# Performance work log

Hardware: AMD Instinct MI355X
Metric: run time of the kernel (lower is better)

## Reference

```python
import jax, jax.numpy as jnp
import numpy as np

HID, NQ, NKV, HD = 4096, 32, 8, 128
EPS = 1e-6
GOLDEN = 1.618033988749895
BASE = 10000.0


def _rmsnorm(x, w, eps=EPS):
    var = jnp.mean(x.astype(jnp.float32) ** 2, axis=-1, keepdims=True)
    return (x * jax.lax.rsqrt(var + eps)).astype(x.dtype) * w


def _rope_half(t, pos, inv_freq):
    # t: (B,T,H,dh); pos: (B,T); inv_freq: (dh//2,)
    ang = pos.astype(jnp.float32)[..., None] * inv_freq  # (B,T,dq)
    cos = jnp.cos(ang)[:, :, None, :]
    sin = jnp.sin(ang)[:, :, None, :]
    dq = inv_freq.shape[0]
    t1, t2 = t[..., :dq], t[..., dq:]
    return jnp.concatenate([t1 * cos - t2 * sin, t1 * sin + t2 * cos], axis=-1)


def _apply_ggrope(q, k, row_ids, col_ids):
    # 2D RoPE: first half of head_dim encodes rows, second half encodes cols;
    # column frequencies scaled by the golden ratio (GGRoPE).
    dh = HD // 2
    inv_freq = 1.0 / (BASE ** (jnp.arange(0, dh, 2, dtype=jnp.float32) / dh))
    inv_freq_col = inv_freq * GOLDEN

    def rot(t):
        tr = _rope_half(t[..., :dh], row_ids, inv_freq)
        tc = _rope_half(t[..., dh:], col_ids, inv_freq_col)
        return jnp.concatenate([tr, tc], axis=-1)

    return rot(q), rot(k)


def setup_inputs() -> dict:
    key = jax.random.key(0)
    ks = jax.random.split(key, 9)
    B, T = 1, 2048
    s = 0.02
    return {
        "x": jax.random.normal(ks[0], (B, T, HID), jnp.float32),
        "row_ids": jax.random.randint(ks[1], (B, T), 0, 30),
        "col_ids": jax.random.randint(ks[2], (B, T), 0, 30),
        "attention_mask": jnp.zeros((B, 1, T, T), jnp.float32),
        "Wq": jax.random.normal(ks[3], (HID, NQ * HD), jnp.float32) * s,
        "Wk": jax.random.normal(ks[4], (HID, NKV * HD), jnp.float32) * s,
        "Wv": jax.random.normal(ks[5], (HID, NKV * HD), jnp.float32) * s,
        "Wo": jax.random.normal(ks[6], (NQ * HD, HID), jnp.float32) * s,
        "q_norm_w": jnp.ones((HD,), jnp.float32),
        "k_norm_w": jnp.ones((HD,), jnp.float32),
    }


def reference(x, row_ids, col_ids, attention_mask, Wq, Wk, Wv, Wo, q_norm_w, k_norm_w):
    B, T, _ = x.shape
    group = NQ // NKV
    q = (x @ Wq).reshape(B, T, NQ, HD)
    k = (x @ Wk).reshape(B, T, NKV, HD)
    v = (x @ Wv).reshape(B, T, NKV, HD)
    q = _rmsnorm(q, q_norm_w)
    k = _rmsnorm(k, k_norm_w)
    q, k = _apply_ggrope(q, k, row_ids, col_ids)
    # expand KV heads to match query heads (GQA)
    k = jnp.repeat(k, group, axis=2)  # (B,T,NQ,HD)
    v = jnp.repeat(v, group, axis=2)
    q = q.transpose(0, 2, 1, 3)  # (B,NQ,T,HD)
    k = k.transpose(0, 2, 1, 3)
    v = v.transpose(0, 2, 1, 3)
    ssmax_scale = (HD ** -0.5) * np.log(max(T, 2)).astype(np.float32)
    scores = jnp.einsum("bhqd,bhkd->bhqk", q, k) * ssmax_scale
    scores = scores + attention_mask
    attn = jax.nn.softmax(scores.astype(jnp.float32), axis=-1).astype(q.dtype)
    out = jnp.einsum("bhqk,bhkd->bhqd", attn, v)
    out = out.transpose(0, 2, 1, 3).reshape(B, T, NQ * HD)
    return out @ Wo
```

## Files before the change

kernel.cpp:

```cpp
#include <hip/hip_runtime.h>
#include <hip/hip_bf16.h>

typedef unsigned short u16;
typedef __attribute__((ext_vector_type(8))) short bf16x8;
typedef __attribute__((ext_vector_type(4))) float f32x4;

#define LOG2E_F 1.4426950408889634f
#define QSCALE (0.08838834764831845f * 7.625595228825695f * 1.4426950408889634f)

__device__ __forceinline__ u16 f2bf(float f) {
  unsigned x = __float_as_uint(f);
  unsigned r = (x + 0x7fffu + ((x >> 16) & 1u)) >> 16;
  return (u16)r;
}
__device__ __forceinline__ float bf2f(u16 u) {
  return __uint_as_float(((unsigned)u) << 16);
}
__device__ __forceinline__ float exp2a(float x) {
  float r;
  asm("v_exp_f32 %0, %1" : "=v"(r) : "v"(x));
  return r;
}
__device__ __forceinline__ unsigned cvtpk(float lo, float hi) {
  unsigned r;
  asm("v_cvt_pk_bf16_f32 %0, %1, %2" : "=v"(r) : "v"(lo), "v"(hi));
  return r;
}

__device__ __forceinline__ void gload_lds16(const void* g, void* l) {
  __builtin_amdgcn_global_load_lds(
      (__attribute__((address_space(1))) void*)(g),
      (__attribute__((address_space(3))) void*)(l), 16, 0, 0);
}

__device__ __forceinline__ f32x4 mfma16(bf16x8 a, bf16x8 b, f32x4 c) {
  return __builtin_amdgcn_mfma_f32_16x16x32_bf16(a, b, c, 0, 0, 0);
}

__global__ __launch_bounds__(256) void cvt_x(const float4* __restrict__ x,
                                             ushort4* __restrict__ xb) {
  size_t i = (size_t)blockIdx.x * 256 + threadIdx.x;
  float4 v = x[i];
  ushort4 o;
  o.x = f2bf(v.x); o.y = f2bf(v.y); o.z = f2bf(v.z); o.w = f2bf(v.w);
  xb[i] = o;
}

__global__ __launch_bounds__(256) void tcvt(const float* __restrict__ src,
                                            u16* __restrict__ dst, int N) {
  __shared__ float t[64][65];
  int bid = blockIdx.x;
  int kt = bid & 63, nt = bid >> 6;
  int k0 = kt * 64, n0 = nt * 64;
  int tid = threadIdx.x;
#pragma unroll
  for (int it = 0; it < 16; ++it) {
    int idx = it * 256 + tid;
    int row = idx >> 6, col = idx & 63;
    t[row][col] = src[(size_t)(k0 + row) * N + n0 + col];
  }
  __syncthreads();
#pragma unroll
  for (int it = 0; it < 8; ++it) {
    int idx = it * 256 + tid;
    int nrow = idx >> 5, kc = idx & 31;
    ushort2 o;
    o.x = f2bf(t[kc * 2][nrow]);
    o.y = f2bf(t[kc * 2 + 1][nrow]);
    *(ushort2*)&dst[(size_t)(n0 + nrow) * 4096 + k0 + kc * 2] = o;
  }
}

__global__ __launch_bounds__(256) void maskflag(const float4* __restrict__ mask,
                                                int* __restrict__ flag) {
  size_t i = (size_t)blockIdx.x * 256 + threadIdx.x;
  float4 v = mask[i];
  if (v.x != 0.f || v.y != 0.f || v.z != 0.f || v.w != 0.f) atomicOr(flag, 1);
}

__global__ __launch_bounds__(256) void trig_kernel(const int* __restrict__ row_ids,
                                                   const int* __restrict__ col_ids,
                                                   float4* __restrict__ trig) {
  int idx = blockIdx.x * 256 + threadIdx.x;
  int tok = idx >> 5, i = idx & 31;
  float inv = exp2f(-(float)i * 0.41524101186092030f);
  float ar = (float)row_ids[tok] * inv;
  float ac = (float)col_ids[tok] * inv * 1.618033988749895f;
  float4 o;
  o.x = cosf(ar); o.y = sinf(ar); o.z = cosf(ac); o.w = sinf(ac);
  trig[idx] = o;
}

__global__ __launch_bounds__(256) void rope_kernel(u16* __restrict__ qk,
                                                   const float4* __restrict__ trig,
                                                   const float* __restrict__ qw,
                                                   const float* __restrict__ kw) {
  const int tok = blockIdx.x;
  const int tid = threadIdx.x;
  const int w = tid >> 6, lane = tid & 63;
  float4 t4 = trig[tok * 32 + (lane & 31)];
  float sgn = (lane < 32) ? -1.0f : 1.0f;

  for (int it = 0; it < 10; ++it) {
    int hh = w + it * 4;
    bool isQ = (hh < 32);
    int colbase = isQ ? hh * 128 : 4096 + (hh - 32) * 128;
    const float* nw = isQ ? qw : kw;
    float scale = isQ ? QSCALE : 1.0f;
    u16* p = qk + (size_t)tok * 5120 + colbase;
    float v1 = bf2f(p[lane]);
    float v2 = bf2f(p[64 + lane]);
    float w1 = nw[lane], w2 = nw[64 + lane];
    float ss = v1 * v1 + v2 * v2;
    ss += __shfl_xor(ss, 1);  ss += __shfl_xor(ss, 2);  ss += __shfl_xor(ss, 4);
    ss += __shfl_xor(ss, 8);  ss += __shfl_xor(ss, 16); ss += __shfl_xor(ss, 32);
    float rinv = rsqrtf(ss * (1.0f / 128.0f) + 1e-6f);
    float n1 = v1 * rinv * w1;
    float n2 = v2 * rinv * w2;
    float p1 = __shfl_xor(n1, 32);
    float p2 = __shfl_xor(n2, 32);
    float r1 = n1 * t4.x + sgn * p1 * t4.y;
    float r2 = n2 * t4.z + sgn * p2 * t4.w;
    p[lane]      = f2bf(r1 * scale);
    p[64 + lane] = f2bf(r2 * scale);
  }
}

template <int MODE>
__global__ __launch_bounds__(512, 2) void gemm256(const u16* __restrict__ A,
                                                  const u16* __restrict__ Bt,
                                                  void* __restrict__ C0,
                                                  u16* __restrict__ Vt, int nnt) {
  extern __shared__ char smem[];
  const int tid = threadIdx.x, lane = tid & 63, w = tid >> 6;
  const int l15 = lane & 15, l4 = lane >> 4;
  const int wr = w >> 2, wc = w & 3;
  constexpr int NF = (MODE == 0) ? 3 : 4;
  constexpr int BNW = (MODE == 0) ? 48 : 64;

  int wgid = (blockIdx.x & 7) * (gridDim.x >> 3) + (blockIdx.x >> 3);
  int kh = 0;
  if (MODE == 1) { kh = wgid >> 7; wgid &= 127; }
  const int mt = wgid / nnt, nt = wgid % nnt;
  const int m0 = mt * 256;
  const int n0 = nt * ((MODE == 0) ? 192 : 256);
  const int tbase = kh * 32;

  const int kswz = (((tid & 7) ^ ((tid >> 3) & 7)) << 4);
  const char* arow = (const char*)A + (size_t)(m0 + (tid >> 3)) * 8192 + kswz;
  const char* brow = (const char*)Bt + (size_t)(n0 + (tid >> 3)) * 8192 + kswz;

  auto stageA = [&](int t, int h) {
#pragma unroll
    for (int rd = 0; rd < 2; ++rd)
      gload_lds16(arow + (size_t)(h * 128 + rd * 64) * 8192 + t * 128,
                  smem + ((t & 1) * 2 + h) * 16384 + rd * 8192 + w * 1024);
  };
  auto stageB0 = [&](int t) {
#pragma unroll
    for (int rd = 0; rd < 3; ++rd)
      gload_lds16(brow + (size_t)(rd * 64) * 8192 + t * 128,
                  smem + 65536 + (t & 1) * 24576 + rd * 8192 + w * 1024);
  };
  auto stageB1 = [&](int t, int h) {
#pragma unroll
    for (int rd = 0; rd < 2; ++rd)
      gload_lds16(brow + (size_t)(h * 128 + rd * 64) * 8192 + t * 128,
                  smem + 65536 + ((t & 1) * 2 + h) * 16384 + rd * 8192 + w * 1024);
  };

  f32x4 acc[8][NF];
#pragma unroll
  for (int i = 0; i < 8; ++i)
#pragma unroll
    for (int j = 0; j < NF; ++j) acc[i][j] = (f32x4){0.f, 0.f, 0.f, 0.f};

  const int aoff0 = ((l4) ^ (l15 & 7)) << 4;
  const int aoff1 = ((4 + l4) ^ (l15 & 7)) << 4;

  stageA(tbase, 0); stageA(tbase, 1);
  if constexpr (MODE == 0) {
    stageB0(tbase); stageB0(tbase + 1);
    asm volatile("s_waitcnt vmcnt(3)" ::: "memory");
  } else {
    stageB1(tbase, 0); stageB1(tbase, 1);
    stageB1(tbase + 1, 0); stageB1(tbase + 1, 1);
    asm volatile("s_waitcnt vmcnt(4)" ::: "memory");
  }
  __builtin_amdgcn_s_barrier();

  auto do_iter = [&](int t0, int last) {
    bf16x8 bfr[NF][2];
#pragma unroll
    for (int p = 0; p < 8; ++p) {
      const int s = p >> 2, qd = p & 3;
      const char* aT = smem + (s * 2 + wr) * 16384 + l15 * 128;
      bf16x8 afr[2][2];
#pragma unroll
      for (int jm = 0; jm < 2; ++jm) {
        afr[jm][0] = *(const bf16x8*)(aT + (2 * qd + jm) * 2048 + aoff0);
        afr[jm][1] = *(const bf16x8*)(aT + (2 * qd + jm) * 2048 + aoff1);
      }
      if (qd == 0) {
        const char* bT;
        if constexpr (MODE == 0)
          bT = smem + 65536 + s * 24576 + (wc * 48 + l15) * 128;
        else
          bT = smem + 65536 + (s * 2 + (wc >> 1)) * 16384 +
               ((wc & 1) * 64 + l15) * 128;
#pragma unroll
        for (int nf = 0; nf < NF; ++nf) {
          bfr[nf][0] = *(const bf16x8*)(bT + nf * 2048 + aoff0);
          bfr[nf][1] = *(const bf16x8*)(bT + nf * 2048 + aoff1);
        }
      }
      if (p == 0) { stageA(t0 + 1, 0); stageA(t0 + 1, 1); }
      if (!last) {
        if constexpr (MODE == 0) {
          if (p == 1) stageB0(t0 + 2);
          if (p == 5) stageB0(t0 + 3);
        } else {
          if (p == 1) stageB1(t0 + 2, 0);
          if (p == 2) stageB1(t0 + 2, 1);
          if (p == 5) stageB1(t0 + 3, 0);
          if (p == 6) stageB1(t0 + 3, 1);
        }
        if (p == 4) { stageA(t0 + 2, 0); stageA(t0 + 2, 1); }
      }
      if (p == 3) {
        if (last) asm volatile("s_waitcnt vmcnt(0)" ::: "memory");
        else if constexpr (MODE == 0)
          asm volatile("s_waitcnt vmcnt(3)" ::: "memory");
        else
          asm volatile("s_waitcnt vmcnt(4)" ::: "memory");
      }
      if (p == 7 && !last) {
        if constexpr (MODE == 0)
          asm volatile("s_waitcnt vmcnt(3)" ::: "memory");
        else
          asm volatile("s_waitcnt vmcnt(4)" ::: "memory");
      }
      __builtin_amdgcn_s_barrier();
      asm volatile("s_waitcnt lgkmcnt(0)" ::: "memory");
      __builtin_amdgcn_sched_barrier(0);
      __builtin_amdgcn_s_setprio(1);
#pragma unroll
      for (int ks = 0; ks < 2; ++ks)
#pragma unroll
        for (int jm = 0; jm < 2; ++jm)
#pragma unroll
          for (int nf = 0; nf < NF; ++nf)
            acc[2 * qd + jm][nf] =
                mfma16(afr[jm][ks], bfr[nf][ks], acc[2 * qd + jm][nf]);
      __builtin_amdgcn_s_setprio(0);
      __builtin_amdgcn_s_barrier();
    }
  };

  constexpr int NIT = (MODE == 0) ? 32 : 16;
  for (int j = 0; j < NIT - 1; ++j) do_iter(tbase + 2 * j, 0);
  do_iter(tbase + 2 * (NIT - 1), 1);

  if (MODE == 0) {
    u16* qkp = (u16*)C0;
#pragma unroll
    for (int mf = 0; mf < 8; ++mf)
#pragma unroll
      for (int nf = 0; nf < NF; ++nf) {
        int ng = n0 + wc * BNW + nf * 16 + l15;
        if (ng < 5120) {
#pragma unroll
          for (int r = 0; r < 4; ++r) {
            int mg = m0 + wr * 128 + mf * 16 + l4 * 4 + r;
            qkp[(size_t)mg * 5120 + ng] = f2bf(acc[mf][nf][r]);
          }
        } else {
          int vr = ng - 5120;
          int mg = m0 + wr * 128 + mf * 16 + l4 * 4;
          ushort4 pk;
          pk.x = f2bf(acc[mf][nf][0]); pk.y = f2bf(acc[mf][nf][1]);
          pk.z = f2bf(acc[mf][nf][2]); pk.w = f2bf(acc[mf][nf][3]);
          *(ushort4*)&Vt[(size_t)vr * 2048 + mg] = pk;
        }
      }
  } else {
    float* Cp = (float*)C0 + (size_t)kh * 8388608;
#pragma unroll
    for (int mf = 0; mf < 8; ++mf)
#pragma unroll
      for (int nf = 0; nf < NF; ++nf) {
        int ng = n0 + wc * BNW + nf * 16 + l15;
#pragma unroll
        for (int r = 0; r < 4; ++r) {
          int mg = m0 + wr * 128 + mf * 16 + l4 * 4 + r;
          Cp[(size_t)mg * 4096 + ng] = acc[mf][nf][r];
        }
      }
  }
}

__global__ __launch_bounds__(256) void reduce2(const float4* __restrict__ p0,
                                               const float4* __restrict__ p1,
                                               float4* __restrict__ out) {
  size_t i = (size_t)blockIdx.x * 256 + threadIdx.x;
  float4 a = p0[i], b = p1[i];
  float4 o;
  o.x = a.x + b.x; o.y = a.y + b.y; o.z = a.z + b.z; o.w = a.w + b.w;
  out[i] = o;
}

__global__ __launch_bounds__(512, 2) void attn_kernel(const u16* __restrict__ qk,
                                                      const u16* __restrict__ vt,
                                                      u16* __restrict__ oat,
                                                      const float* __restrict__ mask,
                                                      const int* __restrict__ flag) {
  __shared__ u16 k_lds[2][64 * 128];
  __shared__ u16 v_lds[2][64 * 128];

  const int tid = threadIdx.x, lane = tid & 63, w = tid >> 6;
  const int l15 = lane & 15, l4 = lane >> 4;
  const int bid = blockIdx.x;
  const int hk = bid & 7;
  const int rest = bid >> 3;
  const int h = hk * 4 + (rest & 3);
  const int qt = rest >> 2;
  const int qbase = qt * 256 + w * 32;

  const bool use_mask = (*flag != 0);
  const char* kbase = (const char*)qk + 8192 + (size_t)hk * 256;
  const char* vbase = (const char*)vt + (size_t)hk * 128 * 4096;

  bf16x8 qf[2][4];
#pragma unroll
  for (int qg = 0; qg < 2; ++qg) {
    const char* qp = (const char*)qk +
                     (size_t)(qbase + qg * 16 + l15) * 10240 + h * 256 + l4 * 16;
#pragma unroll
    for (int ks = 0; ks < 4; ++ks) qf[qg][ks] = *(const bf16x8*)(qp + ks * 64);
  }

  f32x4 oacc[2][8];
#pragma unroll
  for (int qg = 0; qg < 2; ++qg)
#pragma unroll
    for (int fd = 0; fd < 8; ++fd) oacc[qg][fd] = (f32x4){0.f, 0.f, 0.f, 0.f};
  float m_run[2] = {-1e30f, -1e30f};
  float l_run[2] = {0.f, 0.f};

  int koff[4], voff[2];
#pragma unroll
  for (int ks = 0; ks < 4; ++ks) koff[ks] = ((4 * ks + l4) ^ l15) << 4;
#pragma unroll
  for (int ks = 0; ks < 2; ++ks) voff[ks] = ((4 * ks + l4) ^ (l15 & 7)) << 4;

#define STAGE(buf, kv0)                                                        \
  {                                                                            \
    _Pragma("unroll") for (int rd = 0; rd < 2; ++rd) {                         \
      int c = rd * 512 + tid;                                                  \
      int row = c >> 4;                                                        \
      int src = ((c & 15) ^ (row & 15)) << 4;                                  \
      gload_lds16(kbase + (size_t)((kv0) + row) * 10240 + src,                 \
                  (char*)k_lds[buf] + (rd * 512 + w * 64) * 16);               \
      int rowv = c >> 3;                                                       \
      int srcv = ((c & 7) ^ (rowv & 7)) << 4;                                  \
      gload_lds16(vbase + (size_t)rowv * 4096 + (kv0) * 2 + srcv,              \
                  (char*)v_lds[buf] + (rd * 512 + w * 64) * 16);               \
    }                                                                          \
  }

  STAGE(0, 0);
  asm volatile("s_waitcnt vmcnt(0)" ::: "memory");
  __builtin_amdgcn_s_barrier();
  __builtin_amdgcn_sched_barrier(0);

  for (int kt = 0; kt < 32; ++kt) {
    const int cur = kt & 1;
    const int kv0 = kt * 64;
    if (kt < 31) STAGE(cur ^ 1, kv0 + 64);

    f32x4 sA[2][4];
#pragma unroll
    for (int qg = 0; qg < 2; ++qg)
#pragma unroll
      for (int f = 0; f < 4; ++f) sA[qg][f] = (f32x4){0.f, 0.f, 0.f, 0.f};

    __builtin_amdgcn_s_setprio(1);
#pragma unroll
    for (int ks = 0; ks < 4; ++ks) {
      bf16x8 kfr[4];
#pragma unroll
      for (int f = 0; f < 4; ++f)
        kfr[f] = *(const bf16x8*)((const char*)k_lds[cur] +
                                  (16 * f + l15) * 256 + koff[ks]);
#pragma unroll
      for (int f = 0; f < 4; ++f) {
        sA[0][f] = mfma16(kfr[f], qf[0][ks], sA[0][f]);
        sA[1][f] = mfma16(kfr[f], qf[1][ks], sA[1][f]);
      }
    }
    __builtin_amdgcn_s_setprio(0);

    if (use_mask) {
#pragma unroll
      for (int qg = 0; qg < 2; ++qg) {
        int qglob = qbase + qg * 16 + l15;
#pragma unroll
        for (int f = 0; f < 4; ++f)
#pragma unroll
          for (int r = 0; r < 4; ++r) {
            int kvglob = kv0 + 16 * f + 4 * l4 + r;
            sA[qg][f][r] += LOG2E_F * mask[(size_t)qglob * 2048 + kvglob];
          }
      }
    }

    unsigned paw[2][2][4];
#pragma unroll
    for (int qg = 0; qg < 2; ++qg) {
      float mx = fmaxf(fmaxf(fmaxf(sA[qg][0][0], sA[qg][0][1]),
                             fmaxf(sA[qg][0][2], sA[qg][0][3])),
                       fmaxf(fmaxf(sA[qg][1][0], sA[qg][1][1]),
                             fmaxf(sA[qg][1][2], sA[qg][1][3])));
      float mx2 = fmaxf(fmaxf(fmaxf(sA[qg][2][0], sA[qg][2][1]),
                              fmaxf(sA[qg][2][2], sA[qg][2][3])),
                        fmaxf(fmaxf(sA[qg][3][0], sA[qg][3][1]),
                              fmaxf(sA[qg][3][2], sA[qg][3][3])));
      mx = fmaxf(mx, mx2);
      mx = fmaxf(mx, __shfl_xor(mx, 16));
      mx = fmaxf(mx, __shfl_xor(mx, 32));
      if (__any(mx > m_run[qg] + 8.0f)) {
        float mnew = fmaxf(m_run[qg], mx);
        float a = exp2a(m_run[qg] - mnew);
        l_run[qg] *= a;
        m_run[qg] = mnew;
        float a0 = __shfl(a, 4 * l4 + 0);
        float a1 = __shfl(a, 4 * l4 + 1);
        float a2 = __shfl(a, 4 * l4 + 2);
        float a3 = __shfl(a, 4 * l4 + 3);
#pragma unroll
        for (int fd = 0; fd < 8; ++fd) {
          oacc[qg][fd][0] *= a0; oacc[qg][fd][1] *= a1;
          oacc[qg][fd][2] *= a2; oacc[qg][fd][3] *= a3;
        }
      }
      float ps = 0.f;
      unsigned W[4][2];
#pragma unroll
      for (int f = 0; f < 4; ++f) {
        float p0 = exp2a(sA[qg][f][0] - m_run[qg]);
        float p1 = exp2a(sA[qg][f][1] - m_run[qg]);
        float p2 = exp2a(sA[qg][f][2] - m_run[qg]);
        float p3 = exp2a(sA[qg][f][3] - m_run[qg]);
        ps += (p0 + p1) + (p2 + p3);
        W[f][0] = cvtpk(p0, p1);
        W[f][1] = cvtpk(p2, p3);
      }
      ps += __shfl_xor(ps, 16);
      ps += __shfl_xor(ps, 32);
      l_run[qg] += ps;
#pragma unroll
      for (int ks = 0; ks < 2; ++ks)
#pragma unroll
        for (int wd = 0; wd < 4; ++wd) {
          int src = l15 + 16 * (2 * (l4 & 1) + (wd >> 1));
          unsigned v0 = (unsigned)__shfl((int)W[2 * ks][wd & 1], src);
          unsigned v1 = (unsigned)__shfl((int)W[2 * ks + 1][wd & 1], src);
          paw[qg][ks][wd] = (l4 & 2) ? v1 : v0;
        }
    }

    __builtin_amdgcn_s_setprio(1);
#pragma unroll
    for (int ks = 0; ks < 2; ++ks) {
      union { unsigned u[4]; bf16x8 v; } pa0, pa1;
#pragma unroll
      for (int wd = 0; wd < 4; ++wd) {
        pa0.u[wd] = paw[0][ks][wd];
        pa1.u[wd] = paw[1][ks][wd];
      }
#pragma unroll
      for (int fd = 0; fd < 8; ++fd) {
        bf16x8 vb = *(const bf16x8*)((const char*)v_lds[cur] +
                                     (16 * fd + l15) * 128 + voff[ks]);
        oacc[0][fd] = mfma16(pa0.v, vb, oacc[0][fd]);
        oacc[1][fd] = mfma16(pa1.v, vb, oacc[1][fd]);
      }
    }
    __builtin_amdgcn_s_setprio(0);

    if (kt < 31) {
      asm volatile("s_waitcnt vmcnt(0)" ::: "memory");
      __builtin_amdgcn_s_barrier();
      __builtin_amdgcn_sched_barrier(0);
    }
  }

#pragma unroll
  for (int qg = 0; qg < 2; ++qg) {
    float inv[4];
#pragma unroll
    for (int r = 0; r < 4; ++r) inv[r] = 1.0f / __shfl(l_run[qg], 4 * l4 + r);
#pragma unroll
    for (int fd = 0; fd < 8; ++fd) {
      int dg = h * 128 + 16 * fd + l15;
#pragma unroll
      for (int r = 0; r < 4; ++r) {
        int qrow = qbase + qg * 16 + 4 * l4 + r;
        oat[(size_t)qrow * 4096 + dg] = f2bf(oacc[qg][fd][r] * inv[r]);
      }
    }
  }
#undef STAGE
}

extern "C" void kernel_launch(void* const* d_in, const int* in_sizes, int n_in,
                              void* d_out, int out_size, void* d_ws, size_t ws_size,
                              hipStream_t stream) {
  const float* x = (const float*)d_in[0];
  const int* row_ids = (const int*)d_in[1];
  const int* col_ids = (const int*)d_in[2];
  const float* mask = (const float*)d_in[3];
  const float* Wq = (const float*)d_in[4];
  const float* Wk = (const float*)d_in[5];
  const float* Wv = (const float*)d_in[6];
  const float* Wo = (const float*)d_in[7];
  const float* qw = (const float*)d_in[8];
  const float* kw = (const float*)d_in[9];

  char* ws = (char*)d_ws;
  u16* xb      = (u16*)(ws);
  u16* wqkvt   = (u16*)(ws + 16777216);
  u16* wot     = (u16*)(ws + 67108864);
  u16* qkbuf   = (u16*)(ws + 100663296);
  u16* vtbuf   = (u16*)(ws + 121634816);
  u16* oat     = (u16*)(ws + 125829120);
  float4* trig = (float4*)(ws + 142606336);
  int* flag    = (int*)(ws + 143654912);
  float* pbuf  = (float*)(ws);

  hipFuncSetAttribute((const void*)gemm256<0>,
                      hipFuncAttributeMaxDynamicSharedMemorySize, 131072);
  hipFuncSetAttribute((const void*)gemm256<1>,
                      hipFuncAttributeMaxDynamicSharedMemorySize, 131072);

  hipMemsetAsync(flag, 0, 4, stream);
  maskflag<<<4096, 256, 0, stream>>>((const float4*)mask, flag);
  cvt_x<<<8192, 256, 0, stream>>>((const float4*)x, (ushort4*)xb);
  tcvt<<<64 * 64, 256, 0, stream>>>(Wq, wqkvt, 4096);
  tcvt<<<64 * 16, 256, 0, stream>>>(Wk, wqkvt + (size_t)4096 * 4096, 1024);
  tcvt<<<64 * 16, 256, 0, stream>>>(Wv, wqkvt + (size_t)5120 * 4096, 1024);
  tcvt<<<64 * 64, 256, 0, stream>>>(Wo, wot, 4096);
  trig_kernel<<<256, 256, 0, stream>>>(row_ids, col_ids, trig);
  gemm256<0><<<256, 512, 114688, stream>>>(xb, wqkvt, (void*)qkbuf, vtbuf, 32);
  rope_kernel<<<2048, 256, 0, stream>>>(qkbuf, trig, qw, kw);
  attn_kernel<<<256, 512, 0, stream>>>(qkbuf, vtbuf, oat, mask, flag);
  gemm256<1><<<256, 512, 131072, stream>>>(oat, wot, (void*)pbuf, nullptr, 16);
  reduce2<<<8192, 256, 0, stream>>>((const float4*)pbuf,
                                    (const float4*)(pbuf + 8388608),
                                    (float4*)d_out);
}
```

Baseline: 365.1 us.

## Merge preprocessing launches and split attention into smaller 256-thread blocks

The mask check, x conversion and trig-table kernels are merged into one launch, and the four weight transpose-convert launches are merged into another, cutting launch overhead and tail gaps. Separately, the attention kernel moves from 512-thread blocks covering 256 queries to 256-thread blocks covering 128 queries, doubling the grid to 512 blocks for better spread across CUs. Smaller blocks mean each staged K/V tile is reused by fewer query rows, so K/V traffic roughly doubles.

```diff
diff --git a/kernel.cpp b/kernel.cpp
--- a/kernel.cpp
+++ b/kernel.cpp
@@ -37,19 +37,51 @@
   return __builtin_amdgcn_mfma_f32_16x16x32_bf16(a, b, c, 0, 0, 0);
 }
 
-__global__ __launch_bounds__(256) void cvt_x(const float4* __restrict__ x,
-                                             ushort4* __restrict__ xb) {
-  size_t i = (size_t)blockIdx.x * 256 + threadIdx.x;
-  float4 v = x[i];
-  ushort4 o;
-  o.x = f2bf(v.x); o.y = f2bf(v.y); o.z = f2bf(v.z); o.w = f2bf(v.w);
-  xb[i] = o;
-}
-
-__global__ __launch_bounds__(256) void tcvt(const float* __restrict__ src,
-                                            u16* __restrict__ dst, int N) {
+__global__ __launch_bounds__(256) void prep(const float4* __restrict__ x,
+                                            ushort4* __restrict__ xb,
+                                            const float4* __restrict__ mask,
+                                            int* __restrict__ flag,
+                                            const int* __restrict__ row_ids,
+                                            const int* __restrict__ col_ids,
+                                            float4* __restrict__ trig) {
+  int bid = blockIdx.x;
+  if (bid < 8192) {
+    size_t i = (size_t)bid * 256 + threadIdx.x;
+    float4 v = x[i];
+    ushort4 o;
+    o.x = f2bf(v.x); o.y = f2bf(v.y); o.z = f2bf(v.z); o.w = f2bf(v.w);
+    xb[i] = o;
+  } else if (bid < 12288) {
+    size_t i = (size_t)(bid - 8192) * 256 + threadIdx.x;
+    float4 v = mask[i];
+    if (v.x != 0.f || v.y != 0.f || v.z != 0.f || v.w != 0.f) atomicOr(flag, 1);
+  } else {
+    int idx = (bid - 12288) * 256 + threadIdx.x;
+    int tok = idx >> 5, i = idx & 31;
+    float inv = exp2f(-(float)i * 0.41524101186092030f);
+    float ar = (float)row_ids[tok] * inv;
+    float ac = (float)col_ids[tok] * inv * 1.618033988749895f;
+    float4 o;
+    o.x = cosf(ar); o.y = sinf(ar); o.z = cosf(ac); o.w = sinf(ac);
+    trig[idx] = o;
+  }
+}
+
+__global__ __launch_bounds__(256) void tcvt_all(const float* __restrict__ Wq,
+                                                const float* __restrict__ Wk,
+                                                const float* __restrict__ Wv,
+                                                const float* __restrict__ Wo,
+                                                u16* __restrict__ wqkvt,
+                                                u16* __restrict__ wot) {
   __shared__ float t[64][65];
   int bid = blockIdx.x;
+  const float* src;
+  u16* dst;
+  int N;
+  if (bid < 4096)      { src = Wq; dst = wqkvt;                         N = 4096; }
+  else if (bid < 5120) { src = Wk; dst = wqkvt + (size_t)4096 * 4096;   N = 1024; bid -= 4096; }
+  else if (bid < 6144) { src = Wv; dst = wqkvt + (size_t)5120 * 4096;   N = 1024; bid -= 5120; }
+  else                 { src = Wo; dst = wot;                           N = 4096; bid -= 6144; }
   int kt = bid & 63, nt = bid >> 6;
   int k0 = kt * 64, n0 = nt * 64;
   int tid = threadIdx.x;
@@ -69,26 +101,6 @@
     o.y = f2bf(t[kc * 2 + 1][nrow]);
     *(ushort2*)&dst[(size_t)(n0 + nrow) * 4096 + k0 + kc * 2] = o;
   }
-}
-
-__global__ __launch_bounds__(256) void maskflag(const float4* __restrict__ mask,
-                                                int* __restrict__ flag) {
-  size_t i = (size_t)blockIdx.x * 256 + threadIdx.x;
-  float4 v = mask[i];
-  if (v.x != 0.f || v.y != 0.f || v.z != 0.f || v.w != 0.f) atomicOr(flag, 1);
-}
-
-__global__ __launch_bounds__(256) void trig_kernel(const int* __restrict__ row_ids,
-                                                   const int* __restrict__ col_ids,
-                                                   float4* __restrict__ trig) {
-  int idx = blockIdx.x * 256 + threadIdx.x;
-  int tok = idx >> 5, i = idx & 31;
-  float inv = exp2f(-(float)i * 0.41524101186092030f);
-  float ar = (float)row_ids[tok] * inv;
-  float ac = (float)col_ids[tok] * inv * 1.618033988749895f;
-  float4 o;
-  o.x = cosf(ar); o.y = sinf(ar); o.z = cosf(ac); o.w = sinf(ac);
-  trig[idx] = o;
 }
 
 __global__ __launch_bounds__(256) void rope_kernel(u16* __restrict__ qk,
@@ -309,7 +321,7 @@
   out[i] = o;
 }
 
-__global__ __launch_bounds__(512, 2) void attn_kernel(const u16* __restrict__ qk,
+__global__ __launch_bounds__(256, 2) void attn_kernel(const u16* __restrict__ qk,
                                                       const u16* __restrict__ vt,
                                                       u16* __restrict__ oat,
                                                       const float* __restrict__ mask,
@@ -324,7 +336,7 @@
   const int rest = bid >> 3;
   const int h = hk * 4 + (rest & 3);
   const int qt = rest >> 2;
-  const int qbase = qt * 256 + w * 32;
+  const int qbase = qt * 128 + w * 32;
 
   const bool use_mask = (*flag != 0);
   const char* kbase = (const char*)qk + 8192 + (size_t)hk * 256;
@@ -355,16 +367,16 @@
 
 #define STAGE(buf, kv0)                                                        \
   {                                                                            \
-    _Pragma("unroll") for (int rd = 0; rd < 2; ++rd) {                         \
-      int c = rd * 512 + tid;                                                  \
+    _Pragma("unroll") for (int rd = 0; rd < 4; ++rd) {                         \
+      int c = rd * 256 + tid;                                                  \
       int row = c >> 4;                                                        \
       int src = ((c & 15) ^ (row & 15)) << 4;                                  \
       gload_lds16(kbase + (size_t)((kv0) + row) * 10240 + src,                 \
-                  (char*)k_lds[buf] + (rd * 512 + w * 64) * 16);               \
+                  (char*)k_lds[buf] + (rd * 256 + w * 64) * 16);               \
       int rowv = c >> 3;                                                       \
       int srcv = ((c & 7) ^ (rowv & 7)) << 4;                                  \
       gload_lds16(vbase + (size_t)rowv * 4096 + (kv0) * 2 + srcv,              \
-                  (char*)v_lds[buf] + (rd * 512 + w * 64) * 16);               \
+                  (char*)v_lds[buf] + (rd * 256 + w * 64) * 16);               \
     }                                                                          \
   }
 
@@ -544,16 +556,13 @@
                       hipFuncAttributeMaxDynamicSharedMemorySize, 131072);
 
   hipMemsetAsync(flag, 0, 4, stream);
-  maskflag<<<4096, 256, 0, stream>>>((const float4*)mask, flag);
-  cvt_x<<<8192, 256, 0, stream>>>((const float4*)x, (ushort4*)xb);
-  tcvt<<<64 * 64, 256, 0, stream>>>(Wq, wqkvt, 4096);
-  tcvt<<<64 * 16, 256, 0, stream>>>(Wk, wqkvt + (size_t)4096 * 4096, 1024);
-  tcvt<<<64 * 16, 256, 0, stream>>>(Wv, wqkvt + (size_t)5120 * 4096, 1024);
-  tcvt<<<64 * 64, 256, 0, stream>>>(Wo, wot, 4096);
-  trig_kernel<<<256, 256, 0, stream>>>(row_ids, col_ids, trig);
+  prep<<<12544, 256, 0, stream>>>((const float4*)x, (ushort4*)xb,
+                                  (const float4*)mask, flag, row_ids, col_ids,
+                                  trig);
+  tcvt_all<<<10240, 256, 0, stream>>>(Wq, Wk, Wv, Wo, wqkvt, wot);
   gemm256<0><<<256, 512, 114688, stream>>>(xb, wqkvt, (void*)qkbuf, vtbuf, 32);
   rope_kernel<<<2048, 256, 0, stream>>>(qkbuf, trig, qw, kw);
-  attn_kernel<<<256, 512, 0, stream>>>(qkbuf, vtbuf, oat, mask, flag);
+  attn_kernel<<<512, 256, 0, stream>>>(qkbuf, vtbuf, oat, mask, flag);
   gemm256<1><<<256, 512, 131072, stream>>>(oat, wot, (void*)pbuf, nullptr, 16);
   reduce2<<<8192, 256, 0, stream>>>((const float4*)pbuf,
                                     (const float4*)(pbuf + 8388608),
```

New measurement: 346.2 us. 1.05x faster.
